# Kernel tuning notes

Measured on AMD Instinct MI355X. Metric: run time of the kernel, lower is better.

The kernel has to match this reference:

```python
import jax, jax.numpy as jnp
import numpy as np


def setup_inputs() -> dict:
    key = jax.random.key(0)
    k1, k2 = jax.random.split(key)
    B, C, H, W = 64, 512, 28, 28
    x = jax.random.normal(k1, (B, C, H, W), dtype=jnp.float32)
    cc = jax.random.randint(k2, (B, H, W), 0, 2).astype(jnp.bool_)
    return {"x": x, "cc": cc}


def reference(x, cc):
    # x: [B, C, H, W], cc: [B, H, W] bool mask
    m = cc.astype(x.dtype)
    # ave_pool: tmp initialized to x[:, :, 0, 0], then accumulates masked positions
    masked_sum = jnp.einsum('bchw,bhw->bc', x, m) + x[:, :, 0, 0]  # [B, C]
    cnt = jnp.sum(m, axis=(1, 2))                                   # [B]
    denom = jnp.where(cnt == 0, jnp.ones_like(cnt), cnt)            # count==0 -> no division
    mean_pool = masked_sum / denom[:, None]                         # [B, C]
    # AdaptiveMaxPool2d(1): global spatial max
    max_pool = jnp.max(x, axis=(2, 3))                              # [B, C]
    return jnp.concatenate([mean_pool, max_pool], axis=1)           # [B, 2C]
```

## Files before the change

kernel.cpp:

```cpp
#include <hip/hip_runtime.h>


#define HW 784
#define NC 512
#define NB 64

typedef float  vfloat4 __attribute__((ext_vector_type(4)));

__device__ __forceinline__ float dot4(float4 a, float4 b) {
    return a.x * b.x + a.y * b.y + a.z * b.z + a.w * b.w;
}
__device__ __forceinline__ float max4(float4 a) {
    return fmaxf(fmaxf(a.x, a.y), fmaxf(a.z, a.w));
}
__device__ __forceinline__ float sum4(float4 a) {
    return a.x + a.y + a.z + a.w;
}
__device__ __forceinline__ float4 unpack_u8(unsigned int u) {
    return make_float4((float)(u & 0xff), (float)((u >> 8) & 0xff),
                       (float)((u >> 16) & 0xff), (float)((u >> 24) & 0xff));
}
__device__ __forceinline__ float4 ntload4(const float4* p) {
    vfloat4 v = __builtin_nontemporal_load((const vfloat4*)p);
    return make_float4(v.x, v.y, v.z, v.w);
}

__global__ __launch_bounds__(256) void pool_fused_kernel(
    const float* __restrict__ x, const void* __restrict__ cc,
    float* __restrict__ out)
{
    const int blk  = blockIdx.x;
    const int b    = blk >> 4;
    const int grp  = blk & 15;
    const int t    = threadIdx.x;
    const int wave = t >> 6;
    const int lane = t & 63;
    const int c0   = grp * 32 + wave * 8;

    int badInt = 0, badFlt = 0;
    {
        const int4* det = (const int4*)((const unsigned char*)cc + (size_t)b * HW);
        if (lane < 49) {
            int4 d = det[lane];
            badInt = (d.x | d.y | d.z | d.w) & ~1;
            badFlt = (d.x && d.x != 0x3F800000) || (d.y && d.y != 0x3F800000) ||
                     (d.z && d.z != 0x3F800000) || (d.w && d.w != 0x3F800000);
        }
    }
    const bool isInt = !__any(badInt != 0);
    const bool isFlt = !__any(badFlt);

    float4 m0, m1, m2, m3 = make_float4(0.f, 0.f, 0.f, 0.f);
    if (isInt) {
        const int4* mi = (const int4*)cc + (size_t)b * 196;
        int4 a = mi[lane], e = mi[lane + 64], f = mi[lane + 128];
        m0 = make_float4((float)a.x, (float)a.y, (float)a.z, (float)a.w);
        m1 = make_float4((float)e.x, (float)e.y, (float)e.z, (float)e.w);
        m2 = make_float4((float)f.x, (float)f.y, (float)f.z, (float)f.w);
        if (lane < 4) {
            int4 g = mi[lane + 192];
            m3 = make_float4((float)g.x, (float)g.y, (float)g.z, (float)g.w);
        }
    } else if (isFlt) {
        const float4* mf = (const float4*)cc + (size_t)b * 196;
        m0 = mf[lane]; m1 = mf[lane + 64]; m2 = mf[lane + 128];
        if (lane < 4) m3 = mf[lane + 192];
    } else {
        const unsigned int* row =
            (const unsigned int*)((const unsigned char*)cc + (size_t)b * HW);
        m0 = unpack_u8(row[lane]);
        m1 = unpack_u8(row[lane + 64]);
        m2 = unpack_u8(row[lane + 128]);
        if (lane < 4) m3 = unpack_u8(row[lane + 192]);
    }

    float mc = sum4(m0) + sum4(m1) + sum4(m2) + sum4(m3);

    float s[8], mx[8];
#pragma unroll
    for (int j = 0; j < 8; ++j) {
        const float4* xr = (const float4*)(x + (size_t)(b * NC + c0 + j) * HW);
        float4 q0 = ntload4(xr + lane);
        float4 q1 = ntload4(xr + lane + 64);
        float4 q2 = ntload4(xr + lane + 128);
        float sum = dot4(q0, m0) + dot4(q1, m1) + dot4(q2, m2);
        float mm  = fmaxf(fmaxf(max4(q0), max4(q1)), max4(q2));
        if (lane < 4) {
            float4 q3 = ntload4(xr + lane + 192);
            sum += dot4(q3, m3);
            mm = fmaxf(mm, max4(q3));
        }
        if (lane == 0) sum += q0.x;
        s[j] = sum; mx[j] = mm;
    }

    for (int off = 32; off > 0; off >>= 1) {
        mc += __shfl_down(mc, off);
#pragma unroll
        for (int j = 0; j < 8; ++j) {
            s[j] += __shfl_down(s[j], off);
            mx[j] = fmaxf(mx[j], __shfl_down(mx[j], off));
        }
    }

    if (lane == 0) {
        const float inv = 1.0f / ((mc == 0.0f) ? 1.0f : mc);
#pragma unroll
        for (int j = 0; j < 8; ++j) {
            const int c = c0 + j;
            out[(size_t)b * (2 * NC) + c]      = s[j] * inv;
            out[(size_t)b * (2 * NC) + NC + c] = mx[j];
        }
    }
}

extern "C" void kernel_launch(void* const* d_in, const int* in_sizes, int n_in,
                              void* d_out, int out_size, void* d_ws, size_t ws_size,
                              hipStream_t stream) {
    const float* x  = (const float*)d_in[0];
    const void*  cc = d_in[1];
    float* out = (float*)d_out;
    pool_fused_kernel<<<dim3(NB * 16), dim3(256), 0, stream>>>(x, cc, out);
}
```

Baseline: 142.3 us.

## Use butterfly transpose-reduction across channels and simplify mask dtype detection

Replaces the per-channel full-wave shuffle reductions (8 channels × 6 steps × 2 values) with a recursive-halving exchange in which each step folds half the channels onto different lane halves, so fewer shuffles are issued and eight lanes write the results in parallel. Mask-format detection now reads the mask bytes once and reuses them for the uint8 path, with a single int/float path that maps any nonzero word to 1. The tail loads for the last float4 of each row are grouped after the main loop, and launch bounds add an occupancy hint. The kernel is mostly HBM-bound, so the gain from fewer shuffle instructions is likely small.

```diff
diff --git a/kernel.cpp b/kernel.cpp
--- a/kernel.cpp
+++ b/kernel.cpp
@@ -17,15 +17,19 @@
     return a.x + a.y + a.z + a.w;
 }
 __device__ __forceinline__ float4 unpack_u8(unsigned int u) {
-    return make_float4((float)(u & 0xff), (float)((u >> 8) & 0xff),
-                       (float)((u >> 16) & 0xff), (float)((u >> 24) & 0xff));
+    return make_float4((float)(u & 0xffu), (float)((u >> 8) & 0xffu),
+                       (float)((u >> 16) & 0xffu), (float)(u >> 24));
+}
+__device__ __forceinline__ float nz(int v) { return v ? 1.0f : 0.0f; }
+__device__ __forceinline__ float4 unpack_nz(int4 v) {
+    return make_float4(nz(v.x), nz(v.y), nz(v.z), nz(v.w));
 }
 __device__ __forceinline__ float4 ntload4(const float4* p) {
     vfloat4 v = __builtin_nontemporal_load((const vfloat4*)p);
     return make_float4(v.x, v.y, v.z, v.w);
 }
 
-__global__ __launch_bounds__(256) void pool_fused_kernel(
+__global__ __launch_bounds__(256, 4) void pool_fused_kernel(
     const float* __restrict__ x, const void* __restrict__ cc,
     float* __restrict__ out)
 {
@@ -37,80 +41,103 @@
     const int lane = t & 63;
     const int c0   = grp * 32 + wave * 8;
 
-    int badInt = 0, badFlt = 0;
-    {
-        const int4* det = (const int4*)((const unsigned char*)cc + (size_t)b * HW);
-        if (lane < 49) {
-            int4 d = det[lane];
-            badInt = (d.x | d.y | d.z | d.w) & ~1;
-            badFlt = (d.x && d.x != 0x3F800000) || (d.y && d.y != 0x3F800000) ||
-                     (d.z && d.z != 0x3F800000) || (d.w && d.w != 0x3F800000);
-        }
-    }
-    const bool isInt = !__any(badInt != 0);
-    const bool isFlt = !__any(badFlt);
+    const unsigned int* row8 =
+        (const unsigned int*)((const unsigned char*)cc + (size_t)b * HW);
+    unsigned int r0 = row8[lane];
+    unsigned int r1 = row8[lane + 64];
+    unsigned int r2 = row8[lane + 128];
+    unsigned int r3 = (lane < 4) ? row8[lane + 192] : 0u;
+
+    auto not4b = [](unsigned int v) {
+        return (v & 0xFFFFFF00u) != 0u && v != 0x3F800000u;
+    };
+    const bool isU8 = __any(not4b(r0) || not4b(r1) || not4b(r2) || not4b(r3));
 
     float4 m0, m1, m2, m3 = make_float4(0.f, 0.f, 0.f, 0.f);
-    if (isInt) {
+    if (isU8) {
+        m0 = unpack_u8(r0);
+        m1 = unpack_u8(r1);
+        m2 = unpack_u8(r2);
+        if (lane < 4) m3 = unpack_u8(r3);
+    } else {
         const int4* mi = (const int4*)cc + (size_t)b * 196;
-        int4 a = mi[lane], e = mi[lane + 64], f = mi[lane + 128];
-        m0 = make_float4((float)a.x, (float)a.y, (float)a.z, (float)a.w);
-        m1 = make_float4((float)e.x, (float)e.y, (float)e.z, (float)e.w);
-        m2 = make_float4((float)f.x, (float)f.y, (float)f.z, (float)f.w);
-        if (lane < 4) {
-            int4 g = mi[lane + 192];
-            m3 = make_float4((float)g.x, (float)g.y, (float)g.z, (float)g.w);
-        }
-    } else if (isFlt) {
-        const float4* mf = (const float4*)cc + (size_t)b * 196;
-        m0 = mf[lane]; m1 = mf[lane + 64]; m2 = mf[lane + 128];
-        if (lane < 4) m3 = mf[lane + 192];
-    } else {
-        const unsigned int* row =
-            (const unsigned int*)((const unsigned char*)cc + (size_t)b * HW);
-        m0 = unpack_u8(row[lane]);
-        m1 = unpack_u8(row[lane + 64]);
-        m2 = unpack_u8(row[lane + 128]);
-        if (lane < 4) m3 = unpack_u8(row[lane + 192]);
+        m0 = unpack_nz(mi[lane]);
+        m1 = unpack_nz(mi[lane + 64]);
+        m2 = unpack_nz(mi[lane + 128]);
+        if (lane < 4) m3 = unpack_nz(mi[lane + 192]);
     }
 
     float mc = sum4(m0) + sum4(m1) + sum4(m2) + sum4(m3);
 
+    const float4* xr = (const float4*)(x + (size_t)(b * NC + c0) * HW);
     float s[8], mx[8];
 #pragma unroll
     for (int j = 0; j < 8; ++j) {
-        const float4* xr = (const float4*)(x + (size_t)(b * NC + c0 + j) * HW);
-        float4 q0 = ntload4(xr + lane);
-        float4 q1 = ntload4(xr + lane + 64);
-        float4 q2 = ntload4(xr + lane + 128);
+        const float4* xj = xr + j * 196;
+        float4 q0 = ntload4(xj + lane);
+        float4 q1 = ntload4(xj + lane + 64);
+        float4 q2 = ntload4(xj + lane + 128);
         float sum = dot4(q0, m0) + dot4(q1, m1) + dot4(q2, m2);
         float mm  = fmaxf(fmaxf(max4(q0), max4(q1)), max4(q2));
-        if (lane < 4) {
-            float4 q3 = ntload4(xr + lane + 192);
-            sum += dot4(q3, m3);
-            mm = fmaxf(mm, max4(q3));
-        }
         if (lane == 0) sum += q0.x;
         s[j] = sum; mx[j] = mm;
     }
-
-    for (int off = 32; off > 0; off >>= 1) {
-        mc += __shfl_down(mc, off);
+    if (lane < 4) {
 #pragma unroll
         for (int j = 0; j < 8; ++j) {
-            s[j] += __shfl_down(s[j], off);
-            mx[j] = fmaxf(mx[j], __shfl_down(mx[j], off));
+            float4 q3 = ntload4(xr + j * 196 + 192 + lane);
+            s[j] += dot4(q3, m3);
+            mx[j] = fmaxf(mx[j], max4(q3));
         }
     }
 
-    if (lane == 0) {
+#pragma unroll
+    for (int off = 32; off; off >>= 1) mc += __shfl_xor(mc, off);
+
+    const bool h5 = (lane & 32) != 0;
+    float s4[4], y4[4];
+#pragma unroll
+    for (int k = 0; k < 4; ++k) {
+        float sa = s[k]     + __shfl_xor(s[k],     32);
+        float sb = s[k + 4] + __shfl_xor(s[k + 4], 32);
+        s4[k] = h5 ? sb : sa;
+        float ya = fmaxf(mx[k],     __shfl_xor(mx[k],     32));
+        float yb = fmaxf(mx[k + 4], __shfl_xor(mx[k + 4], 32));
+        y4[k] = h5 ? yb : ya;
+    }
+    const bool h4 = (lane & 16) != 0;
+    float s2[2], y2[2];
+#pragma unroll
+    for (int k = 0; k < 2; ++k) {
+        float sa = s4[k]     + __shfl_xor(s4[k],     16);
+        float sb = s4[k + 2] + __shfl_xor(s4[k + 2], 16);
+        s2[k] = h4 ? sb : sa;
+        float ya = fmaxf(y4[k],     __shfl_xor(y4[k],     16));
+        float yb = fmaxf(y4[k + 2], __shfl_xor(y4[k + 2], 16));
+        y2[k] = h4 ? yb : ya;
+    }
+    const bool h3 = (lane & 8) != 0;
+    float s1, y1;
+    {
+        float sa = s2[0] + __shfl_xor(s2[0], 8);
+        float sb = s2[1] + __shfl_xor(s2[1], 8);
+        s1 = h3 ? sb : sa;
+        float ya = fmaxf(y2[0], __shfl_xor(y2[0], 8));
+        float yb = fmaxf(y2[1], __shfl_xor(y2[1], 8));
+        y1 = h3 ? yb : ya;
+    }
+#pragma unroll
+    for (int off = 4; off; off >>= 1) {
+        s1 += __shfl_xor(s1, off);
+        y1 = fmaxf(y1, __shfl_xor(y1, off));
+    }
+
+    if ((lane & 7) == 0) {
+        const int g = lane >> 3;
         const float inv = 1.0f / ((mc == 0.0f) ? 1.0f : mc);
-#pragma unroll
-        for (int j = 0; j < 8; ++j) {
-            const int c = c0 + j;
-            out[(size_t)b * (2 * NC) + c]      = s[j] * inv;
-            out[(size_t)b * (2 * NC) + NC + c] = mx[j];
-        }
+        const int c = c0 + g;
+        out[(size_t)b * (2 * NC) + c]      = s1 * inv;
+        out[(size_t)b * (2 * NC) + NC + c] = y1;
     }
 }
 
```

Result: no change. 142.1 us, median of 2 (-0.1%).
